# Performance work log

Hardware: AMD Instinct MI355X
Metric: run time of the kernel (lower is better)

Reference implementation:

```python
import jax, jax.numpy as jnp
import numpy as np

DIM = 512
HEADS = 8
DIM_HEAD = 64
INNER = HEADS * DIM_HEAD  # 512


def setup_inputs() -> dict:
    key = jax.random.key(0)
    k1, k2, k3, k4 = jax.random.split(key, 4)
    x = jax.random.normal(k1, (2, 2048, DIM), dtype=jnp.float32)
    # nn.Linear weights are [out_features, in_features]
    w_qkv = jax.random.normal(k2, (INNER * 3, DIM), dtype=jnp.float32) * (1.0 / np.sqrt(DIM))
    w_out = jax.random.normal(k3, (DIM, INNER), dtype=jnp.float32) * (1.0 / np.sqrt(INNER))
    b_out = jax.random.normal(k4, (DIM,), dtype=jnp.float32) * 0.01
    return {"x": x, "w_qkv": w_qkv, "w_out": w_out, "b_out": b_out}


def reference(x, w_qkv, w_out, b_out):
    b, n, _ = x.shape
    qkv = x @ w_qkv.T  # (b, n, 3*inner)
    q, k, v = jnp.split(qkv, 3, axis=-1)
    # (b, n, inner) -> (b, h, n, dh)
    def to_heads(t):
        return t.reshape(b, n, HEADS, DIM_HEAD).transpose(0, 2, 1, 3)
    q, k, v = map(to_heads, (q, k, v))
    # Faithful to the torch code: softmax over head dim for q, over seq for k
    q = jax.nn.softmax(q, axis=-1)
    k = jax.nn.softmax(k, axis=-2)
    # torch einsum labels seq as i/j, head dim as d (contracted) -> [n, n] context
    context = jnp.einsum('bhid,bhjd->bhij', k, v)     # (b, h, n, n)
    out = jnp.einsum('bhij,bhie->bhje', context, q)   # (b, h, n, dh)
    out = out.transpose(0, 2, 1, 3).reshape(b, n, INNER)
    return out @ w_out.T + b_out
```

## Files before the change

### kernel.cpp

```cpp
#include <hip/hip_runtime.h>
#include <hip/hip_bf16.h>
#include <math.h>

#define BB   2
#define NN   2048
#define DIMM 512
#define HH   8
#define NC3  1536
#define BN   4096

typedef __attribute__((ext_vector_type(8))) short short8;
typedef __attribute__((ext_vector_type(4))) float f32x4;
typedef unsigned short u16t;

__device__ inline short bfc(float f) {
    __hip_bfloat16 h = __float2bfloat16(f);
    return *reinterpret_cast<short*>(&h);
}
__device__ inline float bf2f(u16t u) {
    return __uint_as_float(((unsigned)u) << 16);
}

#define SWZ(P) ((P) ^ ((((P) >> 7) & 3) << 4))

__device__ inline void gll16(const u16t* gp, void* lp) {
    __builtin_amdgcn_global_load_lds(
        (const __attribute__((address_space(1))) void*)gp,
        (__attribute__((address_space(3))) void*)lp,
        16, 0, 0);
}

__global__ __launch_bounds__(256) void cvt_bf16(
    const float* __restrict__ x, const float* __restrict__ wq,
    u16t* __restrict__ xb, u16t* __restrict__ wqb)
{
    int t = blockIdx.x * 256 + threadIdx.x;
    const float4* src; ushort4* dst; int i;
    if (t < 524288) { src = (const float4*)x;  dst = (ushort4*)xb;  i = t; }
    else            { src = (const float4*)wq; dst = (ushort4*)wqb; i = t - 524288; }
    float4 v = src[i];
    ushort4 u;
    u.x = (u16t)bfc(v.x); u.y = (u16t)bfc(v.y);
    u.z = (u16t)bfc(v.z); u.w = (u16t)bfc(v.w);
    dst[i] = u;
}

__global__ __launch_bounds__(256) void qkvgemm(
    const u16t* __restrict__ A, const u16t* __restrict__ Bw,
    u16t* __restrict__ QKV, float* __restrict__ Mm)
{
    __shared__ __align__(16) char smem[32768];

    const int tid  = threadIdx.x;
    const int wave = tid >> 6, lane = tid & 63;
    const int wr = wave >> 1, wc = wave & 1;

    int bid = blockIdx.x;
    if (bid < 64) {
        f32x4 z = (f32x4){0.f, 0.f, 0.f, 0.f};
        ((f32x4*)Mm)[bid * 256 + tid] = z;
    }
    const int row0 = ((bid & 7) * 4 + ((bid >> 3) & 3)) * 128;
    const int c0   = (bid >> 5) * 128;

    size_t gA[2], gB[2];
#pragma unroll
    for (int j = 0; j < 2; ++j) {
        int c = wave * 2 + j;
        int X = (c * 64 + lane) * 16;
        int gi = SWZ(X) >> 4;
        int row = gi >> 2, col = (gi & 3) * 8;
        gA[j] = (size_t)(row0 + row) * DIMM + col;
        gB[j] = (size_t)(c0   + row) * DIMM + col;
    }

    int rdA[4], rdB[4];
#pragma unroll
    for (int i = 0; i < 4; ++i) {
        int Pa = (wr * 64 + i * 16 + (lane & 15)) * 64 + (lane >> 4) * 16;
        rdA[i] = SWZ(Pa);
        int Pb = (wc * 64 + i * 16 + (lane & 15)) * 64 + (lane >> 4) * 16;
        rdB[i] = 8192 + SWZ(Pb);
    }

#define QSTAGE(BUF, KT) {                                                     \
    char* sb = smem + (BUF) * 16384;                                          \
    _Pragma("unroll")                                                         \
    for (int j = 0; j < 2; ++j) {                                             \
        gll16(A  + gA[j] + (KT), sb + (wave * 2 + j) * 1024);                 \
        gll16(Bw + gB[j] + (KT), sb + 8192 + (wave * 2 + j) * 1024);          \
    } }

    f32x4 acc[4][4];
#pragma unroll
    for (int i = 0; i < 4; ++i)
#pragma unroll
        for (int j = 0; j < 4; ++j) acc[i][j] = (f32x4){0.f, 0.f, 0.f, 0.f};

    QSTAGE(0, 0);
    for (int t = 0; t < 16; ++t) {
        __syncthreads();
        if (t < 15) QSTAGE((t + 1) & 1, (t + 1) * 32);
        const char* rb = smem + (t & 1) * 16384;
        short8 af[4], bfr[4];
#pragma unroll
        for (int i = 0; i < 4; ++i) {
            af[i]  = *(const short8*)(rb + rdA[i]);
            bfr[i] = *(const short8*)(rb + rdB[i]);
        }
#pragma unroll
        for (int i = 0; i < 4; ++i)
#pragma unroll
            for (int j = 0; j < 4; ++j)
                acc[i][j] = __builtin_amdgcn_mfma_f32_16x16x32_bf16(
                    af[i], bfr[j], acc[i][j], 0, 0, 0);
    }
#undef QSTAGE

#pragma unroll
    for (int j = 0; j < 4; ++j) {
        int col = c0 + wc * 64 + j * 16 + (lane & 15);
#pragma unroll
        for (int i = 0; i < 4; ++i) {
#pragma unroll
            for (int r = 0; r < 4; ++r) {
                int row = row0 + wr * 64 + i * 16 + (lane >> 4) * 4 + r;
                QKV[(size_t)row * NC3 + col] = (u16t)bfc(acc[i][j][r]);
            }
        }
    }
}

#define TST 136

__global__ __launch_bounds__(512) void mpart(
    const u16t* __restrict__ QKV, float* __restrict__ Mm, float* __restrict__ ksump)
{
    __shared__ __align__(16) char sh[34816];
    u16t* ksT = (u16t*)sh;
    u16t* qsT = (u16t*)(sh + 17408);

    const int bh = blockIdx.x, ch = blockIdx.y;
    const int b = bh >> 3, h = bh & 7;
    const int tid = threadIdx.x;
    const u16t* base = QKV + ((size_t)b * NN + ch * 128) * NC3 + h * 64;

    const int k7 = tid & 7;
    const int d0 = k7 * 8;
    const int rr = tid >> 3;

#pragma unroll
    for (int pass = 0; pass < 2; ++pass) {
        int r = pass * 64 + rr;
        const u16t* rowp = base + (size_t)r * NC3 + d0;
        short8 qv = *(const short8*)(rowp);
        short8 kv = *(const short8*)(rowp + 512);
        float e[8]; float s = 0.f;
#pragma unroll
        for (int u = 0; u < 8; ++u) { e[u] = __expf(bf2f((u16t)qv[u])); s += e[u]; }
        s += __shfl_xor(s, 1); s += __shfl_xor(s, 2); s += __shfl_xor(s, 4);
        float inv = 1.0f / s;
        int gx = ((r >> 3) ^ k7) * 8 + (r & 7);
#pragma unroll
        for (int u = 0; u < 8; ++u)
            qsT[(d0 + u) * TST + gx] = (u16t)bfc(e[u] * inv);
#pragma unroll
        for (int u = 0; u < 8; ++u)
            ksT[(d0 + u) * TST + gx] = (u16t)bfc(__expf(bf2f((u16t)kv[u])));
    }
    __syncthreads();

    if (tid < 64) {
        float kss = 0.f;
#pragma unroll
        for (int gg = 0; gg < 16; ++gg) {
            short8 v = *(const short8*)(ksT + tid * TST + gg * 8);
#pragma unroll
            for (int u = 0; u < 8; ++u) kss += bf2f((u16t)v[u]);
        }
        ksump[(bh * 16 + ch) * 64 + tid] = kss;
    }

    const int wave = tid >> 6, lane = tid & 63;
    const int g = wave >> 1, kh = wave & 1;
    const int dl = lane & 15, kq = lane >> 4;
    const int d = g * 16 + dl;

    f32x4 acc[4];
#pragma unroll
    for (int j = 0; j < 4; ++j) acc[j] = (f32x4){0.f, 0.f, 0.f, 0.f};

#pragma unroll
    for (int ks2 = 0; ks2 < 2; ++ks2) {
        int kb = kh * 64 + ks2 * 32 + kq * 8;
        short8 af = *(const short8*)(ksT + d * TST + ((((kb >> 3) ^ (d >> 3))) << 3));
#pragma unroll
        for (int j = 0; j < 4; ++j) {
            int e = j * 16 + dl;
            short8 bfrj = *(const short8*)(qsT + e * TST + ((((kb >> 3) ^ (e >> 3))) << 3));
            acc[j] = __builtin_amdgcn_mfma_f32_16x16x32_bf16(af, bfrj, acc[j], 0, 0, 0);
        }
    }

    float* mm = Mm + (size_t)bh * 4096;
#pragma unroll
    for (int j = 0; j < 4; ++j)
#pragma unroll
        for (int r = 0; r < 4; ++r)
            atomicAdd(&mm[(g * 16 + kq * 4 + r) * 64 + j * 16 + dl], acc[j][r]);
}

__global__ __launch_bounds__(256) void w2t(
    const float* __restrict__ Mm, const float* __restrict__ ksump,
    const float* __restrict__ w_out, u16t* __restrict__ W2T)
{
    __shared__ float kst[64];
    __shared__ float Ms[64][68];
    __shared__ float Wt[32][68];

    const int bh = blockIdx.x, ot = blockIdx.y;
    const int b = bh >> 3, h = bh & 7;
    const int tid = threadIdx.x;
    const int d = tid & 63, og = tid >> 6;
    const int ob = ot * 32;

    if (tid < 64) {
        float s = 0.f;
#pragma unroll
        for (int c = 0; c < 16; ++c) s += ksump[(bh * 16 + c) * 64 + tid];
        kst[tid] = s;
    }
#pragma unroll
    for (int it = 0; it < 4; ++it) {
        int idx4 = it * 256 + tid;
        int dd = idx4 >> 4, e4 = idx4 & 15;
        *(float4*)&Ms[dd][e4 * 4] =
            *(const float4*)(Mm + (size_t)bh * 4096 + idx4 * 4);
    }
    {
        int o = tid >> 3, e0 = (tid & 7) * 8;
        *(float4*)&Wt[o][e0] =
            *(const float4*)&w_out[(size_t)(ob + o) * DIMM + h * 64 + e0];
        *(float4*)&Wt[o][e0 + 4] =
            *(const float4*)&w_out[(size_t)(ob + o) * DIMM + h * 64 + e0 + 4];
    }
    __syncthreads();

    float Mreg[64];
#pragma unroll
    for (int e4 = 0; e4 < 16; ++e4) {
        float4 v = *(const float4*)&Ms[d][e4 * 4];
        Mreg[e4 * 4 + 0] = v.x; Mreg[e4 * 4 + 1] = v.y;
        Mreg[e4 * 4 + 2] = v.z; Mreg[e4 * 4 + 3] = v.w;
    }
    float inv = 1.0f / kst[d];

#pragma unroll
    for (int oo = 0; oo < 8; ++oo) {
        int o = og * 8 + oo;
        float a = 0.f;
#pragma unroll
        for (int e4 = 0; e4 < 16; ++e4) {
            float4 wv = *(const float4*)&Wt[o][e4 * 4];
            a += wv.x * Mreg[e4 * 4 + 0] + wv.y * Mreg[e4 * 4 + 1]
               + wv.z * Mreg[e4 * 4 + 2] + wv.w * Mreg[e4 * 4 + 3];
        }
        W2T[((size_t)b * DIMM + ob + o) * DIMM + h * 64 + d] = (u16t)bfc(a * inv);
    }
}

__global__ __launch_bounds__(256) void outgemm(
    const u16t* __restrict__ Aq, const u16t* __restrict__ W2T,
    const float* __restrict__ bias, float* __restrict__ Out)
{
    __shared__ __align__(16) char smem[24576];

    const int tid  = threadIdx.x;
    const int wave = tid >> 6, lane = tid & 63;
    const int wr = wave >> 1, wc = wave & 1;

    int bid = blockIdx.x;
    const int row0 = ((bid & 7) * 4 + ((bid >> 3) & 3)) * 128;
    const int c0   = (bid >> 5) * 64;
    const u16t* Bp = W2T + (size_t)(row0 >> 11) * (DIMM * DIMM);

    size_t gA[2], gB;
#pragma unroll
    for (int j = 0; j < 2; ++j) {
        int c = wave * 2 + j;
        int gi = SWZ((c * 64 + lane) * 16) >> 4;
        int row = gi >> 2, col = (gi & 3) * 8;
        gA[j] = (size_t)(row0 + row) * NC3 + col;
    }
    {
        int gi = SWZ((wave * 64 + lane) * 16) >> 4;
        int row = gi >> 2, col = (gi & 3) * 8;
        gB = (size_t)(c0 + row) * DIMM + col;
    }

    int rdA[4], rdB[2];
#pragma unroll
    for (int i = 0; i < 4; ++i) {
        int Pa = (wr * 64 + i * 16 + (lane & 15)) * 64 + (lane >> 4) * 16;
        rdA[i] = SWZ(Pa);
    }
#pragma unroll
    for (int j = 0; j < 2; ++j) {
        int Pb = (wc * 32 + j * 16 + (lane & 15)) * 64 + (lane >> 4) * 16;
        rdB[j] = 8192 + SWZ(Pb);
    }

#define OSTAGE(BUF, KT) {                                                     \
    char* sb = smem + (BUF) * 12288;                                          \
    _Pragma("unroll")                                                         \
    for (int j = 0; j < 2; ++j)                                               \
        gll16(Aq + gA[j] + (KT), sb + (wave * 2 + j) * 1024);                 \
    gll16(Bp + gB + (KT), sb + 8192 + wave * 1024);                           \
    }

    f32x4 acc[4][2];
#pragma unroll
    for (int i = 0; i < 4; ++i)
#pragma unroll
        for (int j = 0; j < 2; ++j) acc[i][j] = (f32x4){0.f, 0.f, 0.f, 0.f};

    OSTAGE(0, 0);
    for (int t = 0; t < 16; ++t) {
        __syncthreads();
        if (t < 15) OSTAGE((t + 1) & 1, (t + 1) * 32);
        const char* rb = smem + (t & 1) * 12288;
        short8 af[4], bfr[2];
#pragma unroll
        for (int i = 0; i < 4; ++i) af[i]  = *(const short8*)(rb + rdA[i]);
#pragma unroll
        for (int j = 0; j < 2; ++j) bfr[j] = *(const short8*)(rb + rdB[j]);
#pragma unroll
        for (int i = 0; i < 4; ++i)
#pragma unroll
            for (int j = 0; j < 2; ++j)
                acc[i][j] = __builtin_amdgcn_mfma_f32_16x16x32_bf16(
                    af[i], bfr[j], acc[i][j], 0, 0, 0);
    }
#undef OSTAGE

#pragma unroll
    for (int j = 0; j < 2; ++j) {
        int col = c0 + wc * 32 + j * 16 + (lane & 15);
        float bb = bias[col];
#pragma unroll
        for (int i = 0; i < 4; ++i) {
#pragma unroll
            for (int r = 0; r < 4; ++r) {
                int row = row0 + wr * 64 + i * 16 + (lane >> 4) * 4 + r;
                Out[(size_t)row * DIMM + col] = acc[i][j][r] + bb;
            }
        }
    }
}

extern "C" void kernel_launch(void* const* d_in, const int* in_sizes, int n_in,
                              void* d_out, int out_size, void* d_ws, size_t ws_size,
                              hipStream_t stream)
{
    const float* x     = (const float*)d_in[0];
    const float* w_qkv = (const float*)d_in[1];
    const float* w_out = (const float*)d_in[2];
    const float* b_out = (const float*)d_in[3];
    float* out = (float*)d_out;

    char* w = (char*)d_ws;
    u16t*  xb   = (u16t*) (w);
    u16t*  wqb  = (u16t*) (w + 4194304);
    u16t*  QKV  = (u16t*) (w + 5767168);
    float* Mm   = (float*)(w + 18350080);
    float* ksum = (float*)(w + 18612224);
    u16t*  W2T  = (u16t*) (w + 18677760);

    cvt_bf16<<<dim3(2816), 256, 0, stream>>>(x, w_qkv, xb, wqb);

    qkvgemm<<<dim3(384), 256, 0, stream>>>(xb, wqb, QKV, Mm);

    mpart<<<dim3(16, 16), 512, 0, stream>>>(QKV, Mm, ksum);

    w2t<<<dim3(16, 16), 256, 0, stream>>>(Mm, ksum, w_out, W2T);

    outgemm<<<dim3(256), 256, 0, stream>>>(QKV + 1024, W2T, b_out, out);
}
```

Measured before the change: 48.07 us.

## Fuse fp32-to-bf16 conversion into QKV GEMM via fp32 LDS staging

Removes the separate cvt_bf16 kernel and has qkvgemm load fp32 x and w_qkv directly into LDS with global_load_lds, converting to bf16 in registers before the MFMA. LDS usage doubles to 64KB with a new XOR swizzle for fp32 rows, and the block-to-tile mapping is reordered. This saves a kernel launch and an extra global round trip for the bf16 copies. In exchange the GEMM moves twice the bytes into LDS, repeats the conversion work across tiles, and lower occupancy may hurt latency hiding.

```diff
diff --git a/kernel.cpp b/kernel.cpp
--- a/kernel.cpp
+++ b/kernel.cpp
@@ -29,27 +29,18 @@
         (__attribute__((address_space(3))) void*)lp,
         16, 0, 0);
 }
-
-__global__ __launch_bounds__(256) void cvt_bf16(
-    const float* __restrict__ x, const float* __restrict__ wq,
-    u16t* __restrict__ xb, u16t* __restrict__ wqb)
-{
-    int t = blockIdx.x * 256 + threadIdx.x;
-    const float4* src; ushort4* dst; int i;
-    if (t < 524288) { src = (const float4*)x;  dst = (ushort4*)xb;  i = t; }
-    else            { src = (const float4*)wq; dst = (ushort4*)wqb; i = t - 524288; }
-    float4 v = src[i];
-    ushort4 u;
-    u.x = (u16t)bfc(v.x); u.y = (u16t)bfc(v.y);
-    u.z = (u16t)bfc(v.z); u.w = (u16t)bfc(v.w);
-    dst[i] = u;
+__device__ inline void gllf(const float* gp, void* lp) {
+    __builtin_amdgcn_global_load_lds(
+        (const __attribute__((address_space(1))) void*)gp,
+        (__attribute__((address_space(3))) void*)lp,
+        16, 0, 0);
 }
 
 __global__ __launch_bounds__(256) void qkvgemm(
-    const u16t* __restrict__ A, const u16t* __restrict__ Bw,
+    const float* __restrict__ A, const float* __restrict__ Bw,
     u16t* __restrict__ QKV, float* __restrict__ Mm)
 {
-    __shared__ __align__(16) char smem[32768];
+    __shared__ __align__(16) char smem[65536];
 
     const int tid  = threadIdx.x;
     const int wave = tid >> 6, lane = tid & 63;
@@ -60,36 +51,45 @@
         f32x4 z = (f32x4){0.f, 0.f, 0.f, 0.f};
         ((f32x4*)Mm)[bid * 256 + tid] = z;
     }
-    const int row0 = ((bid & 7) * 4 + ((bid >> 3) & 3)) * 128;
-    const int c0   = (bid >> 5) * 128;
-
-    size_t gA[2], gB[2];
-#pragma unroll
-    for (int j = 0; j < 2; ++j) {
-        int c = wave * 2 + j;
-        int X = (c * 64 + lane) * 16;
-        int gi = SWZ(X) >> 4;
-        int row = gi >> 2, col = (gi & 3) * 8;
-        gA[j] = (size_t)(row0 + row) * DIMM + col;
-        gB[j] = (size_t)(c0   + row) * DIMM + col;
-    }
-
-    int rdA[4], rdB[4];
+    const int x = bid & 7, k = bid >> 3;
+    const int row0 = ((x & 3) * 8 + (k & 7)) * 128;
+    const int c0   = ((x >> 2) * 6 + (k >> 3)) * 128;
+
+    size_t gAo[4], gBo[4];
+#pragma unroll
+    for (int j = 0; j < 4; ++j) {
+        int c = wave * 4 + j;
+        int rl = c * 8 + (lane >> 3);
+        int gs = (lane & 7) ^ (lane >> 3);
+        gAo[j] = (size_t)(row0 + rl) * DIMM + gs * 4;
+        gBo[j] = (size_t)(c0   + rl) * DIMM + gs * 4;
+    }
+
+    int aA0[4], aA1[4], aB0[4], aB1[4];
+    const int g0 = (lane >> 4) * 2;
 #pragma unroll
     for (int i = 0; i < 4; ++i) {
-        int Pa = (wr * 64 + i * 16 + (lane & 15)) * 64 + (lane >> 4) * 16;
-        rdA[i] = SWZ(Pa);
-        int Pb = (wc * 64 + i * 16 + (lane & 15)) * 64 + (lane >> 4) * 16;
-        rdB[i] = 8192 + SWZ(Pb);
+        int ra = wr * 64 + i * 16 + (lane & 15);
+        aA0[i] = ra * 128 + (((g0    ) ^ (ra & 7)) << 4);
+        aA1[i] = ra * 128 + (((g0 + 1) ^ (ra & 7)) << 4);
+        int rb2 = wc * 64 + i * 16 + (lane & 15);
+        aB0[i] = 16384 + rb2 * 128 + (((g0    ) ^ (rb2 & 7)) << 4);
+        aB1[i] = 16384 + rb2 * 128 + (((g0 + 1) ^ (rb2 & 7)) << 4);
     }
 
 #define QSTAGE(BUF, KT) {                                                     \
-    char* sb = smem + (BUF) * 16384;                                          \
+    char* sb = smem + (BUF) * 32768;                                          \
     _Pragma("unroll")                                                         \
-    for (int j = 0; j < 2; ++j) {                                             \
-        gll16(A  + gA[j] + (KT), sb + (wave * 2 + j) * 1024);                 \
-        gll16(Bw + gB[j] + (KT), sb + 8192 + (wave * 2 + j) * 1024);          \
+    for (int j = 0; j < 4; ++j) {                                             \
+        gllf(A  + gAo[j] + (KT), sb + (wave * 4 + j) * 1024);                 \
+        gllf(Bw + gBo[j] + (KT), sb + 16384 + (wave * 4 + j) * 1024);         \
     } }
+
+#define CVT8(FR, LO, HI) {                                                    \
+    FR[0] = bfc((LO).x); FR[1] = bfc((LO).y);                                 \
+    FR[2] = bfc((LO).z); FR[3] = bfc((LO).w);                                 \
+    FR[4] = bfc((HI).x); FR[5] = bfc((HI).y);                                 \
+    FR[6] = bfc((HI).z); FR[7] = bfc((HI).w); }
 
     f32x4 acc[4][4];
 #pragma unroll
@@ -101,12 +101,16 @@
     for (int t = 0; t < 16; ++t) {
         __syncthreads();
         if (t < 15) QSTAGE((t + 1) & 1, (t + 1) * 32);
-        const char* rb = smem + (t & 1) * 16384;
+        const char* rb = smem + (t & 1) * 32768;
         short8 af[4], bfr[4];
 #pragma unroll
         for (int i = 0; i < 4; ++i) {
-            af[i]  = *(const short8*)(rb + rdA[i]);
-            bfr[i] = *(const short8*)(rb + rdB[i]);
+            float4 lo = *(const float4*)(rb + aA0[i]);
+            float4 hi = *(const float4*)(rb + aA1[i]);
+            CVT8(af[i], lo, hi);
+            float4 lob = *(const float4*)(rb + aB0[i]);
+            float4 hib = *(const float4*)(rb + aB1[i]);
+            CVT8(bfr[i], lob, hib);
         }
 #pragma unroll
         for (int i = 0; i < 4; ++i)
@@ -116,6 +120,7 @@
                     af[i], bfr[j], acc[i][j], 0, 0, 0);
     }
 #undef QSTAGE
+#undef CVT8
 
 #pragma unroll
     for (int j = 0; j < 4; ++j) {
@@ -369,16 +374,12 @@
     float* out = (float*)d_out;
 
     char* w = (char*)d_ws;
-    u16t*  xb   = (u16t*) (w);
-    u16t*  wqb  = (u16t*) (w + 4194304);
-    u16t*  QKV  = (u16t*) (w + 5767168);
-    float* Mm   = (float*)(w + 18350080);
-    float* ksum = (float*)(w + 18612224);
-    u16t*  W2T  = (u16t*) (w + 18677760);
-
-    cvt_bf16<<<dim3(2816), 256, 0, stream>>>(x, w_qkv, xb, wqb);
-
-    qkvgemm<<<dim3(384), 256, 0, stream>>>(xb, wqb, QKV, Mm);
+    u16t*  QKV  = (u16t*) (w);
+    float* Mm   = (float*)(w + 12582912);
+    float* ksum = (float*)(w + 12845056);
+    u16t*  W2T  = (u16t*) (w + 12910592);
+
+    qkvgemm<<<dim3(384), 256, 0, stream>>>(x, w_qkv, QKV, Mm);
 
     mpart<<<dim3(16, 16), 512, 0, stream>>>(QKV, Mm, ksum);
 
```

After: 49.83 us. 3.7% more time.
